# Optimization experiments

Hardware: AMD Instinct MI355X
Metric: run time of the kernel (lower is better)

The kernel has to match this reference:

```python
import jax, jax.numpy as jnp
import numpy as np

VOXEL = 0.1          # superpoint_voxel_size
NUM_BATCHES = 4      # B (batch indices in coords[:,0] are in [0, B))


def setup_inputs() -> dict:
    key = jax.random.key(0)
    k1, k2, k3, k4, k5, k6, k7 = jax.random.split(key, 7)
    N, D = 1_000_000, 64
    batch_ids = jax.random.randint(k1, (N,), 0, NUM_BATCHES).astype(jnp.float32)
    xyz = jax.random.uniform(k2, (N, 3), dtype=jnp.float32) * 50.0  # 50m scene
    coords = jnp.concatenate([batch_ids[:, None], xyz], axis=1)      # (N,4)
    features = jax.random.normal(k3, (N, D), dtype=jnp.float32)
    s1 = 1.0 / np.sqrt(3.0)
    s2 = 1.0 / np.sqrt(D)
    W1 = jax.random.uniform(k4, (3, D), minval=-s1, maxval=s1, dtype=jnp.float32)
    b1 = jax.random.uniform(k5, (D,), minval=-s1, maxval=s1, dtype=jnp.float32)
    W2 = jax.random.uniform(k6, (D, D), minval=-s2, maxval=s2, dtype=jnp.float32)
    b2 = jax.random.uniform(k7, (D,), minval=-s2, maxval=s2, dtype=jnp.float32)
    return {"coords": coords, "features": features, "W1": W1, "b1": b1, "W2": W2, "b2": b2}


def reference(coords, features, W1, b1, W2, b2):
    N, D = features.shape
    batch_ids = coords[:, 0].astype(jnp.int32)          # (N,)
    xyz = coords[:, 1:4]                                 # (N,3)
    q = jnp.floor(xyz / VOXEL).astype(jnp.int32)         # voxel quantization
    combined = jnp.concatenate([batch_ids[:, None], q], axis=1)  # (N,4) int32 keys

    # torch.unique(dim=0, return_inverse=True): lexicographically sorted unique
    # rows. We pad to a fixed S=N segments (fill rows sorted to the tail via a
    # max sentinel); `valid` masks out the padding.
    SENT = jnp.iinfo(jnp.int32).max
    unique_sp, sp_to_point = jnp.unique(
        combined, axis=0, size=N, fill_value=SENT, return_inverse=True)
    sp_to_point = sp_to_point.reshape(-1)                # (N,)

    counts = jax.ops.segment_sum(jnp.ones((N,), jnp.float32), sp_to_point, num_segments=N)
    valid = counts > 0
    c = jnp.maximum(counts, 1.0)[:, None]                # clamp(min=1)

    sp_features = jax.ops.segment_sum(features, sp_to_point, num_segments=N) / c  # (N,D) mean
    sp_centers = jax.ops.segment_sum(xyz, sp_to_point, num_segments=N) / c        # (N,3) mean

    # pos_enc: Linear(3,D) -> ReLU -> Linear(D,D)
    pos = jnp.maximum(sp_centers @ W1 + b1, 0.0) @ W2 + b2
    sp_features = jnp.where(valid[:, None], sp_features + pos, 0.0)
    sp_centers = jnp.where(valid[:, None], sp_centers, 0.0)

    # batch_offsets: cumulative superpoint counts per batch (padding -> dump bin B)
    sp_batch = jnp.where(valid, unique_sp[:, 0], NUM_BATCHES)
    per_batch = jax.ops.segment_sum(jnp.ones((N,), jnp.int32), sp_batch,
                                    num_segments=NUM_BATCHES + 1)[:NUM_BATCHES]
    batch_offsets = jnp.concatenate([jnp.zeros((1,), jnp.int32), jnp.cumsum(per_batch)])
    return sp_features, sp_centers, sp_to_point, batch_offsets
```

## Files before the change

### kernel.cpp

```cpp
#include <hip/hip_runtime.h>
#include <stdint.h>


static constexpr uint32_t NWORDS = 1u << 24;
static constexpr uint32_t NBLK   = NWORDS / 1024;
static constexpr uint32_t MCAP   = 65536;

typedef __attribute__((ext_vector_type(8))) short short8;
typedef __attribute__((ext_vector_type(4))) float f32x4;

__device__ __forceinline__ short f2bf(float x) {
    union { float f; uint32_t u; } v; v.f = x;
    uint32_t u = v.u;
    uint32_t r = (u + 0x7FFFu + ((u >> 16) & 1u)) >> 16;
    return (short)r;
}

__device__ __forceinline__ uint32_t point_key(float4 c) {
    uint32_t b  = (uint32_t)(int)c.x;
    uint32_t qx = (uint32_t)(int)floorf(c.y / 0.1f);
    uint32_t qy = (uint32_t)(int)floorf(c.z / 0.1f);
    uint32_t qz = (uint32_t)(int)floorf(c.w / 0.1f);
    return (b << 27) | (qx << 18) | (qy << 9) | qz;
}

__global__ void k0_w2t(const float* __restrict__ W2, short* __restrict__ W2T) {
    int t = blockIdx.x * 256 + threadIdx.x;
    if (t < 4096) {
        int col = t >> 6, k = t & 63;
        W2T[col * 64 + k] = f2bf(W2[k * 64 + col]);
    }
}

__global__ void k1_keys(const float4* __restrict__ coords, uint32_t* __restrict__ bitmap, int N) {
    int i = blockIdx.x * blockDim.x + threadIdx.x;
    if (i >= N) return;
    uint32_t key = point_key(coords[i]);
    atomicOr(&bitmap[key >> 5], 1u << (key & 31u));
}

__global__ __launch_bounds__(256) void k2a_blockscan(
        const uint4* __restrict__ bm4, uint16_t* __restrict__ scan4,
        uint32_t* __restrict__ bsum) {
    int t = threadIdx.x;
    int lane = t & 63, wid = t >> 6;
    uint4 v = bm4[(size_t)blockIdx.x * 256 + t];
    uint32_t pc = __popc(v.x) + __popc(v.y) + __popc(v.z) + __popc(v.w);
    uint32_t sc = pc;
    #pragma unroll
    for (int off = 1; off < 64; off <<= 1) {
        uint32_t n = __shfl_up(sc, off);
        if (lane >= off) sc += n;
    }
    __shared__ uint32_t wt[4];
    if (lane == 63) wt[wid] = sc;
    __syncthreads();
    uint32_t wbase = 0;
    #pragma unroll
    for (int w = 0; w < 4; ++w) wbase += (w < wid) ? wt[w] : 0u;
    scan4[(size_t)blockIdx.x * 256 + t] = (uint16_t)(wbase + sc - pc);
    if (t == 255) bsum[blockIdx.x] = wbase + sc;
}

__global__ void k2b_topscan(const uint32_t* __restrict__ bsum, uint32_t* __restrict__ bscan) {
    __shared__ uint32_t s[1024];
    int t = threadIdx.x;
    uint32_t base = (uint32_t)t * 16u;
    const uint4* b4 = (const uint4*)(bsum + base);
    uint32_t sum = 0;
    #pragma unroll
    for (int k = 0; k < 4; ++k) { uint4 v = b4[k]; sum += v.x + v.y + v.z + v.w; }
    s[t] = sum;
    __syncthreads();
    for (int off = 1; off < 1024; off <<= 1) {
        uint32_t v = (t >= off) ? s[t - off] : 0u;
        __syncthreads();
        s[t] += v;
        __syncthreads();
    }
    uint32_t run = s[t] - sum;
    for (int k = 0; k < 16; ++k) { bscan[base + k] = run; run += bsum[base + k]; }
    if (t == 1023) bscan[16384] = run;
}

__global__ void k3a_rank(const float4* __restrict__ coords,
                         uint32_t* __restrict__ ranks,
                         const uint32_t* __restrict__ bitmap,
                         const uint16_t* __restrict__ scan4,
                         const uint32_t* __restrict__ bscan,
                         float* __restrict__ psum,
                         uint32_t* __restrict__ mctr,
                         float* __restrict__ msum,
                         float* __restrict__ mfeat,
                         float* __restrict__ out_sp, int N) {
    int i = blockIdx.x * blockDim.x + threadIdx.x;
    if (i >= N) return;
    float4 c = coords[i];
    uint32_t key = point_key(c);
    uint32_t w = key >> 5, bit = key & 31u;
    uint4 q = *(const uint4*)(bitmap + (w & ~3u));
    uint32_t wd[4] = {q.x, q.y, q.z, q.w};
    uint32_t idx = w & 3u;
    uint32_t r = bscan[w >> 10] + (uint32_t)scan4[w >> 2];
    uint32_t cur = 0;
    #pragma unroll
    for (uint32_t j = 0; j < 4; ++j) {
        r += (j < idx) ? __popc(wd[j]) : 0u;
        cur = (j == idx) ? wd[j] : cur;
    }
    r += __popc(cur & ((1u << bit) - 1u));
    ranks[i] = r;
    out_sp[i] = (float)r;
    float* p = psum + 8u * (size_t)r;
    float old = atomicAdd(p, 1.0f);
    *(float4*)(p + 4) = make_float4(c.y, c.z, c.w, __uint_as_float((uint32_t)i));
    if (old == 1.0f) {
        uint32_t slot = atomicAdd(mctr, 1u);
        if (slot < MCAP) {
            *(uint32_t*)(p + 1) = slot + 1u;
            float4 z = make_float4(0.f, 0.f, 0.f, 0.f);
            *(float4*)(msum + 4u * (size_t)slot) = z;
            float4* fz = (float4*)(mfeat + 64u * (size_t)slot);
            #pragma unroll
            for (int qq = 0; qq < 16; ++qq) fz[qq] = z;
        }
    }
}

__global__ void k3fix(const float4* __restrict__ coords,
                      const float* __restrict__ features,
                      const uint32_t* __restrict__ ranks,
                      const float4* __restrict__ psum4,
                      float* __restrict__ msum,
                      float* __restrict__ mfeat, int N) {
    int i = blockIdx.x * blockDim.x + threadIdx.x;
    if (i >= N) return;
    uint32_t r = ranks[i];
    float4 q0 = psum4[2 * (size_t)r];
    uint32_t sl = __float_as_uint(q0.y);
    if (sl == 0) return;
    sl -= 1u;
    float cnt = q0.x;
    float4 c = coords[i];
    float* m = msum + 4u * (size_t)sl;
    atomicAdd(m + 0, c.y);
    atomicAdd(m + 1, c.z);
    atomicAdd(m + 2, c.w);
    float iv = 1.0f / cnt;
    const float* frow = features + (size_t)i * 64;
    float* orow = mfeat + (size_t)sl * 64;
    #pragma unroll 1
    for (int qq = 0; qq < 64; ++qq) atomicAdd(&orow[qq], frow[qq] * iv);
}

__global__ __launch_bounds__(256) void k5_fused(
        const f32x4* __restrict__ features4,
        const float4* __restrict__ psum4,
        const float4* __restrict__ msum,
        const f32x4* __restrict__ mfeat4,
        const float* __restrict__ W1, const float* __restrict__ b1,
        const short* __restrict__ W2T, const float* __restrict__ b2,
        f32x4* __restrict__ out_feat4, float* __restrict__ out_cent, int N) {
    int lane = threadIdx.x & 63;
    int rows_base = blockIdx.x * 256 + (threadIdx.x >> 6) * 64;

    float cntg[4], scx[4], scy[4], scz[4];
    uint32_t invg[4], slotg[4];
    #pragma unroll
    for (int g = 0; g < 4; ++g) {
        int rg = rows_base + (g << 4) + (lane & 15);
        int rgc = rg < N ? rg : N - 1;
        float4 q0 = psum4[2 * (size_t)rgc];
        float4 q1 = psum4[2 * (size_t)rgc + 1];
        float cnt = q0.x;
        cntg[g] = cnt;
        slotg[g] = __float_as_uint(q0.y);
        invg[g] = __float_as_uint(q1.w);
        float sx = q1.x, sy = q1.y, sz = q1.z;
        if (cnt > 1.5f) {
            float4 m = msum[slotg[g] - 1u];
            sx = m.x; sy = m.y; sz = m.z;
        }
        float ic = cnt > 0.f ? 1.f / cnt : 0.f;
        scx[g] = sx * ic; scy[g] = sy * ic; scz[g] = sz * ic;
    }

    int my = rows_base + lane;
    if (my < N) {
        float4 q0 = psum4[2 * (size_t)my];
        float4 q1 = psum4[2 * (size_t)my + 1];
        float cnt = q0.x;
        float sx = q1.x, sy = q1.y, sz = q1.z;
        if (cnt > 1.5f) {
            float4 m = msum[__float_as_uint(q0.y) - 1u];
            sx = m.x; sy = m.y; sz = m.z;
        }
        float ic = cnt > 0.f ? 1.f / cnt : 0.f;
        out_cent[3 * (size_t)my + 0] = sx * ic;
        out_cent[3 * (size_t)my + 1] = sy * ic;
        out_cent[3 * (size_t)my + 2] = sz * ic;
    }

    f32x4 acc[4][4];
    #pragma unroll
    for (int cg = 0; cg < 4; ++cg) {
        f32x4 bv = ((const f32x4*)b2)[(cg << 2) + (lane >> 4)];
        #pragma unroll
        for (int g = 0; g < 4; ++g)
            acc[g][cg] = bv;
    }

    #pragma unroll
    for (int s = 0; s < 2; ++s) {
        int kb = s * 32 + ((lane >> 4) << 3);
        float4 tx0 = *(const float4*)(W1 + kb),       tx1 = *(const float4*)(W1 + kb + 4);
        float4 ty0 = *(const float4*)(W1 + 64 + kb),  ty1 = *(const float4*)(W1 + 64 + kb + 4);
        float4 tz0 = *(const float4*)(W1 + 128 + kb), tz1 = *(const float4*)(W1 + 128 + kb + 4);
        float4 tb0 = *(const float4*)(b1 + kb),       tb1 = *(const float4*)(b1 + kb + 4);
        float w1x[8] = {tx0.x, tx0.y, tx0.z, tx0.w, tx1.x, tx1.y, tx1.z, tx1.w};
        float w1y[8] = {ty0.x, ty0.y, ty0.z, ty0.w, ty1.x, ty1.y, ty1.z, ty1.w};
        float w1z[8] = {tz0.x, tz0.y, tz0.z, tz0.w, tz1.x, tz1.y, tz1.z, tz1.w};
        float b1v[8] = {tb0.x, tb0.y, tb0.z, tb0.w, tb1.x, tb1.y, tb1.z, tb1.w};

        short8 afrag[4];
        #pragma unroll
        for (int cg = 0; cg < 4; ++cg) {
            int col = (cg << 4) | (lane & 15);
            afrag[cg] = *(const short8*)(W2T + col * 64 + kb);
        }

        #pragma unroll
        for (int g = 0; g < 4; ++g) {
            short8 hf;
            #pragma unroll
            for (int j = 0; j < 8; ++j) {
                float h = fmaf(scz[g], w1z[j], fmaf(scy[g], w1y[j], fmaf(scx[g], w1x[j], b1v[j])));
                hf[j] = f2bf(fmaxf(h, 0.0f));
            }
            #pragma unroll
            for (int cg = 0; cg < 4; ++cg)
                acc[g][cg] = __builtin_amdgcn_mfma_f32_16x16x32_bf16(afrag[cg], hf, acc[g][cg], 0, 0, 0);
        }
    }

    #pragma unroll
    for (int g = 0; g < 4; ++g) {
        int gr = rows_base + (g << 4) + (lane & 15);
        if (gr >= N) continue;
        float cnt = cntg[g];
        f32x4 v[4];
        #pragma unroll
        for (int cg = 0; cg < 4; ++cg) v[cg] = acc[g][cg];
        if (cnt == 0.0f) {
            #pragma unroll
            for (int cg = 0; cg < 4; ++cg) v[cg] = (f32x4){0.f, 0.f, 0.f, 0.f};
        } else if (cnt == 1.0f) {
            size_t fb = (size_t)invg[g] * 16 + (lane >> 4);
            #pragma unroll
            for (int cg = 0; cg < 4; ++cg) v[cg] += features4[fb + (cg << 2)];
        } else {
            size_t mb = (size_t)(slotg[g] - 1u) * 16 + (lane >> 4);
            #pragma unroll
            for (int cg = 0; cg < 4; ++cg) v[cg] += mfeat4[mb + (cg << 2)];
        }
        size_t ob = (size_t)gr * 16 + (lane >> 4);
        #pragma unroll
        for (int cg = 0; cg < 4; ++cg)
            out_feat4[ob + (cg << 2)] = v[cg];
    }
}

__global__ void k6_offsets(const uint32_t* __restrict__ bscan, float* __restrict__ out_off) {
    int t = threadIdx.x;
    if (t < 5) {
        uint32_t v;
        if (t == 0)      v = 0u;
        else if (t == 4) v = bscan[16384];
        else             v = bscan[(uint32_t)t << 12];
        out_off[t] = (float)v;
    }
}

extern "C" void kernel_launch(void* const* d_in, const int* in_sizes, int n_in,
                              void* d_out, int out_size, void* d_ws, size_t ws_size,
                              hipStream_t stream) {
    const float4* coords = (const float4*)d_in[0];
    const float*  feats  = (const float*)d_in[1];
    const float*  W1 = (const float*)d_in[2];
    const float*  b1 = (const float*)d_in[3];
    const float*  W2 = (const float*)d_in[4];
    const float*  b2 = (const float*)d_in[5];
    int N = in_sizes[0] / 4;

    char* ws = (char*)d_ws;
    size_t o = 0;
    uint32_t* bitmap = (uint32_t*)(ws + o); o += (size_t)NWORDS * 4;
    uint16_t* scan4  = (uint16_t*)(ws + o); o += (size_t)(NWORDS / 4) * 2;
    uint32_t* bsum   = (uint32_t*)(ws + o); o += (size_t)NBLK * 4;
    uint32_t* bscan  = (uint32_t*)(ws + o); o += (size_t)(NBLK + 1) * 4;
    o = (o + 31) & ~(size_t)31;
    float*    psum   = (float*)(ws + o);    o += (size_t)N * 32;
    uint32_t* ranks  = (uint32_t*)(ws + o); o += (size_t)N * 4;
    o = (o + 15) & ~(size_t)15;
    short*    W2T    = (short*)(ws + o);    o += 8192;
    uint32_t* mctr   = (uint32_t*)(ws + o); o += 16;
    float*    msum   = (float*)(ws + o);    o += (size_t)MCAP * 16;
    float*    mfeat  = (float*)(ws + o);    o += (size_t)MCAP * 256;

    float* out_feat = (float*)d_out;
    float* out_cent = out_feat + (size_t)N * 64;
    float* out_sp   = out_cent + (size_t)N * 3;
    float* out_off  = out_sp + N;

    hipMemsetAsync(bitmap, 0, (size_t)NWORDS * 4, stream);
    hipMemsetAsync(psum, 0, (size_t)N * 32, stream);
    hipMemsetAsync(mctr, 0, 16, stream);

    int nb = (N + 255) / 256;
    k0_w2t<<<16, 256, 0, stream>>>(W2, W2T);
    k1_keys<<<nb, 256, 0, stream>>>(coords, bitmap, N);
    k2a_blockscan<<<NBLK, 256, 0, stream>>>((const uint4*)bitmap, scan4, bsum);
    k2b_topscan<<<1, 1024, 0, stream>>>(bsum, bscan);
    k3a_rank<<<nb, 256, 0, stream>>>(coords, ranks, bitmap, scan4, bscan, psum,
                                     mctr, msum, mfeat, out_sp, N);
    k3fix<<<nb, 256, 0, stream>>>(coords, feats, ranks, (const float4*)psum, msum, mfeat, N);
    k5_fused<<<nb, 256, 0, stream>>>((const f32x4*)feats, (const float4*)psum,
                                     (const float4*)msum, (const f32x4*)mfeat,
                                     W1, b1, W2T, b2, (f32x4*)out_feat, out_cent, N);
    k6_offsets<<<1, 64, 0, stream>>>(bscan, out_off);
}
```

Baseline: 337.3 us.

## Fuse multi-point scatter into point-order MLP kernel and scatter singleton outputs

Merges the k3fix accumulation pass into a point-ordered kernel that computes the positional MLP from each point's own coordinates and writes singleton superpoint rows directly to their rank position. A second kernel handles empty rows and the rare multi-point superpoints with a scalar per-wavefront MLP, and writes the centers. This removes one full pass over ranks and coords and makes feature reads sequential. In exchange, output writes become a scatter by rank, and the multi-point path uses slower scalar FP32 math.

```diff
diff --git a/kernel.cpp b/kernel.cpp
--- a/kernel.cpp
+++ b/kernel.cpp
@@ -113,7 +113,7 @@
     out_sp[i] = (float)r;
     float* p = psum + 8u * (size_t)r;
     float old = atomicAdd(p, 1.0f);
-    *(float4*)(p + 4) = make_float4(c.y, c.z, c.w, __uint_as_float((uint32_t)i));
+    *(float4*)(p + 4) = make_float4(c.y, c.z, c.w, 0.f);
     if (old == 1.0f) {
         uint32_t slot = atomicAdd(mctr, 1u);
         if (slot < MCAP) {
@@ -127,78 +127,46 @@
     }
 }
 
-__global__ void k3fix(const float4* __restrict__ coords,
-                      const float* __restrict__ features,
-                      const uint32_t* __restrict__ ranks,
-                      const float4* __restrict__ psum4,
-                      float* __restrict__ msum,
-                      float* __restrict__ mfeat, int N) {
-    int i = blockIdx.x * blockDim.x + threadIdx.x;
-    if (i >= N) return;
-    uint32_t r = ranks[i];
-    float4 q0 = psum4[2 * (size_t)r];
-    uint32_t sl = __float_as_uint(q0.y);
-    if (sl == 0) return;
-    sl -= 1u;
-    float cnt = q0.x;
-    float4 c = coords[i];
-    float* m = msum + 4u * (size_t)sl;
-    atomicAdd(m + 0, c.y);
-    atomicAdd(m + 1, c.z);
-    atomicAdd(m + 2, c.w);
-    float iv = 1.0f / cnt;
-    const float* frow = features + (size_t)i * 64;
-    float* orow = mfeat + (size_t)sl * 64;
-    #pragma unroll 1
-    for (int qq = 0; qq < 64; ++qq) atomicAdd(&orow[qq], frow[qq] * iv);
-}
-
-__global__ __launch_bounds__(256) void k5_fused(
+__global__ __launch_bounds__(256) void k5a_scatter(
+        const float4* __restrict__ coords,
         const f32x4* __restrict__ features4,
+        const uint32_t* __restrict__ ranks,
         const float4* __restrict__ psum4,
-        const float4* __restrict__ msum,
-        const f32x4* __restrict__ mfeat4,
+        float* __restrict__ msum, float* __restrict__ mfeat,
         const float* __restrict__ W1, const float* __restrict__ b1,
         const short* __restrict__ W2T, const float* __restrict__ b2,
-        f32x4* __restrict__ out_feat4, float* __restrict__ out_cent, int N) {
+        f32x4* __restrict__ out_feat4, int N) {
     int lane = threadIdx.x & 63;
-    int rows_base = blockIdx.x * 256 + (threadIdx.x >> 6) * 64;
-
-    float cntg[4], scx[4], scy[4], scz[4];
-    uint32_t invg[4], slotg[4];
+    int base = blockIdx.x * 256 + (threadIdx.x >> 6) * 64;
+    int i = base + lane;
+    int icl = i < N ? i : N - 1;
+    float4 c = coords[icl];
+    uint32_t r = ranks[icl];
+    float4 q0 = psum4[2 * (size_t)r];
+    float cnt = q0.x;
+
+    if (i < N && cnt > 1.5f) {
+        uint32_t slw = __float_as_uint(q0.y);
+        if (slw) {
+            uint32_t sl = slw - 1u;
+            float* m = msum + 4u * (size_t)sl;
+            atomicAdd(m + 0, c.y);
+            atomicAdd(m + 1, c.z);
+            atomicAdd(m + 2, c.w);
+            float iv = 1.0f / cnt;
+            const float* frow = (const float*)(features4 + (size_t)icl * 16);
+            float* orow = mfeat + (size_t)sl * 64;
+            #pragma unroll 1
+            for (int qq = 0; qq < 64; ++qq) atomicAdd(&orow[qq], frow[qq] * iv);
+        }
+    }
+
+    float scx[4], scy[4], scz[4];
     #pragma unroll
     for (int g = 0; g < 4; ++g) {
-        int rg = rows_base + (g << 4) + (lane & 15);
-        int rgc = rg < N ? rg : N - 1;
-        float4 q0 = psum4[2 * (size_t)rgc];
-        float4 q1 = psum4[2 * (size_t)rgc + 1];
-        float cnt = q0.x;
-        cntg[g] = cnt;
-        slotg[g] = __float_as_uint(q0.y);
-        invg[g] = __float_as_uint(q1.w);
-        float sx = q1.x, sy = q1.y, sz = q1.z;
-        if (cnt > 1.5f) {
-            float4 m = msum[slotg[g] - 1u];
-            sx = m.x; sy = m.y; sz = m.z;
-        }
-        float ic = cnt > 0.f ? 1.f / cnt : 0.f;
-        scx[g] = sx * ic; scy[g] = sy * ic; scz[g] = sz * ic;
-    }
-
-    int my = rows_base + lane;
-    if (my < N) {
-        float4 q0 = psum4[2 * (size_t)my];
-        float4 q1 = psum4[2 * (size_t)my + 1];
-        float cnt = q0.x;
-        float sx = q1.x, sy = q1.y, sz = q1.z;
-        if (cnt > 1.5f) {
-            float4 m = msum[__float_as_uint(q0.y) - 1u];
-            sx = m.x; sy = m.y; sz = m.z;
-        }
-        float ic = cnt > 0.f ? 1.f / cnt : 0.f;
-        out_cent[3 * (size_t)my + 0] = sx * ic;
-        out_cent[3 * (size_t)my + 1] = sy * ic;
-        out_cent[3 * (size_t)my + 2] = sz * ic;
+        int pg = base + (g << 4) + (lane & 15);
+        float4 cc = coords[pg < N ? pg : N - 1];
+        scx[g] = cc.y; scy[g] = cc.z; scz[g] = cc.w;
     }
 
     f32x4 acc[4][4];
@@ -245,28 +213,69 @@
 
     #pragma unroll
     for (int g = 0; g < 4; ++g) {
-        int gr = rows_base + (g << 4) + (lane & 15);
-        if (gr >= N) continue;
-        float cnt = cntg[g];
-        f32x4 v[4];
-        #pragma unroll
-        for (int cg = 0; cg < 4; ++cg) v[cg] = acc[g][cg];
-        if (cnt == 0.0f) {
+        int src = (g << 4) | (lane & 15);
+        int prow = base + src;
+        float cr = __shfl(cnt, src);
+        uint32_t rr = (uint32_t)__shfl((int)r, src);
+        if (prow < N && cr == 1.0f) {
+            size_t fb = (size_t)prow * 16 + (lane >> 4);
+            size_t ob = (size_t)rr * 16 + (lane >> 4);
             #pragma unroll
-            for (int cg = 0; cg < 4; ++cg) v[cg] = (f32x4){0.f, 0.f, 0.f, 0.f};
-        } else if (cnt == 1.0f) {
-            size_t fb = (size_t)invg[g] * 16 + (lane >> 4);
-            #pragma unroll
-            for (int cg = 0; cg < 4; ++cg) v[cg] += features4[fb + (cg << 2)];
-        } else {
-            size_t mb = (size_t)(slotg[g] - 1u) * 16 + (lane >> 4);
-            #pragma unroll
-            for (int cg = 0; cg < 4; ++cg) v[cg] += mfeat4[mb + (cg << 2)];
-        }
-        size_t ob = (size_t)gr * 16 + (lane >> 4);
-        #pragma unroll
-        for (int cg = 0; cg < 4; ++cg)
-            out_feat4[ob + (cg << 2)] = v[cg];
+            for (int cg = 0; cg < 4; ++cg)
+                out_feat4[ob + (cg << 2)] = acc[g][cg] + features4[fb + (cg << 2)];
+        }
+    }
+}
+
+__global__ __launch_bounds__(256) void k5b_finish(
+        const float4* __restrict__ psum4,
+        const float4* __restrict__ msum,
+        const float* __restrict__ mfeat,
+        const float* __restrict__ W1, const float* __restrict__ b1,
+        const float* __restrict__ W2, const float* __restrict__ b2,
+        float* __restrict__ out_feat, float* __restrict__ out_cent, int N) {
+    int lane = threadIdx.x & 63;
+    int r = blockIdx.x * 256 + threadIdx.x;
+    int wrbase = blockIdx.x * 256 + (threadIdx.x & ~63);
+    int rcl = r < N ? r : N - 1;
+    float4 q0 = psum4[2 * (size_t)rcl];
+    float4 q1 = psum4[2 * (size_t)rcl + 1];
+    float cnt = r < N ? q0.x : 1.0f;
+    uint32_t slw = __float_as_uint(q0.y);
+
+    float cx = q1.x, cy = q1.y, cz = q1.z;
+    bool multi = (cnt > 1.5f) && (slw != 0u);
+    if (multi) {
+        float4 m = msum[slw - 1u];
+        float iv = 1.0f / cnt;
+        cx = m.x * iv; cy = m.y * iv; cz = m.z * iv;
+    }
+    if (r < N) {
+        bool valid = cnt > 0.0f;
+        out_cent[3 * (size_t)r + 0] = valid ? cx : 0.f;
+        out_cent[3 * (size_t)r + 1] = valid ? cy : 0.f;
+        out_cent[3 * (size_t)r + 2] = valid ? cz : 0.f;
+    }
+
+    unsigned long long zm = __ballot(r < N && cnt == 0.0f);
+    while (zm) {
+        int src = __ffsll(zm) - 1; zm &= zm - 1;
+        out_feat[(size_t)(wrbase + src) * 64 + lane] = 0.0f;
+    }
+
+    unsigned long long mm = __ballot(r < N && multi);
+    while (mm) {
+        int src = __ffsll(mm) - 1; mm &= mm - 1;
+        float mcx = __shfl(cx, src), mcy = __shfl(cy, src), mcz = __shfl(cz, src);
+        uint32_t msl = (uint32_t)__shfl((int)(slw - 1u), src);
+        float out = b2[lane];
+        #pragma unroll 1
+        for (int k = 0; k < 64; ++k) {
+            float hk = fmaxf(b1[k] + mcx * W1[k] + mcy * W1[64 + k] + mcz * W1[128 + k], 0.0f);
+            out = fmaf(hk, W2[64 * k + lane], out);
+        }
+        out += mfeat[(size_t)msl * 64 + lane];
+        out_feat[(size_t)(wrbase + src) * 64 + lane] = out;
     }
 }
 
@@ -323,9 +332,10 @@
     k2b_topscan<<<1, 1024, 0, stream>>>(bsum, bscan);
     k3a_rank<<<nb, 256, 0, stream>>>(coords, ranks, bitmap, scan4, bscan, psum,
                                      mctr, msum, mfeat, out_sp, N);
-    k3fix<<<nb, 256, 0, stream>>>(coords, feats, ranks, (const float4*)psum, msum, mfeat, N);
-    k5_fused<<<nb, 256, 0, stream>>>((const f32x4*)feats, (const float4*)psum,
-                                     (const float4*)msum, (const f32x4*)mfeat,
-                                     W1, b1, W2T, b2, (f32x4*)out_feat, out_cent, N);
+    k5a_scatter<<<nb, 256, 0, stream>>>(coords, (const f32x4*)feats, ranks,
+                                        (const float4*)psum, msum, mfeat,
+                                        W1, b1, W2T, b2, (f32x4*)out_feat, N);
+    k5b_finish<<<nb, 256, 0, stream>>>((const float4*)psum, (const float4*)msum,
+                                       mfeat, W1, b1, W2, b2, out_feat, out_cent, N);
     k6_offsets<<<1, 64, 0, stream>>>(bscan, out_off);
 }
```

Result: slower. 367.7 us (+9.0%).

## Compact multi-point voxels into a list so the fix-up kernel skips singletons

Applied to the files above, without the earlier changes.

The rank kernel now appends every point that lands in an already-occupied voxel to a compact list through an atomic counter, flagging the second arrival. The fix-up kernel walks only that list with a small grid-stride launch instead of reading ranks and psum for all N points. It also adds the first point's contribution via its stored index. The cost is an extra global atomic counter plus list writes, and possible contention on that counter. Correctness now depends on the first point's write racing with the second point's atomic.

```diff
diff --git a/kernel.cpp b/kernel.cpp
--- a/kernel.cpp
+++ b/kernel.cpp
@@ -89,9 +89,10 @@
                          const uint16_t* __restrict__ scan4,
                          const uint32_t* __restrict__ bscan,
                          float* __restrict__ psum,
-                         uint32_t* __restrict__ mctr,
+                         uint32_t* __restrict__ ctrs,
                          float* __restrict__ msum,
                          float* __restrict__ mfeat,
+                         uint2* __restrict__ mlist,
                          float* __restrict__ out_sp, int N) {
     int i = blockIdx.x * blockDim.x + threadIdx.x;
     if (i >= N) return;
@@ -113,44 +114,64 @@
     out_sp[i] = (float)r;
     float* p = psum + 8u * (size_t)r;
     float old = atomicAdd(p, 1.0f);
-    *(float4*)(p + 4) = make_float4(c.y, c.z, c.w, __uint_as_float((uint32_t)i));
-    if (old == 1.0f) {
-        uint32_t slot = atomicAdd(mctr, 1u);
-        if (slot < MCAP) {
-            *(uint32_t*)(p + 1) = slot + 1u;
-            float4 z = make_float4(0.f, 0.f, 0.f, 0.f);
-            *(float4*)(msum + 4u * (size_t)slot) = z;
-            float4* fz = (float4*)(mfeat + 64u * (size_t)slot);
-            #pragma unroll
-            for (int qq = 0; qq < 16; ++qq) fz[qq] = z;
-        }
-    }
-}
-
-__global__ void k3fix(const float4* __restrict__ coords,
-                      const float* __restrict__ features,
-                      const uint32_t* __restrict__ ranks,
-                      const float4* __restrict__ psum4,
-                      float* __restrict__ msum,
-                      float* __restrict__ mfeat, int N) {
-    int i = blockIdx.x * blockDim.x + threadIdx.x;
-    if (i >= N) return;
-    uint32_t r = ranks[i];
-    float4 q0 = psum4[2 * (size_t)r];
-    uint32_t sl = __float_as_uint(q0.y);
-    if (sl == 0) return;
-    sl -= 1u;
-    float cnt = q0.x;
-    float4 c = coords[i];
+    if (old == 0.0f) {
+        *(float4*)(p + 4) = make_float4(c.y, c.z, c.w, __uint_as_float((uint32_t)i));
+    } else {
+        bool alloc = (old == 1.0f);
+        if (alloc) {
+            uint32_t slot = atomicAdd(&ctrs[0], 1u);
+            if (slot < MCAP) {
+                *(uint32_t*)(p + 1) = slot + 1u;
+                float4 z = make_float4(0.f, 0.f, 0.f, 0.f);
+                *(float4*)(msum + 4u * (size_t)slot) = z;
+                float4* fz = (float4*)(mfeat + 64u * (size_t)slot);
+                #pragma unroll
+                for (int qq = 0; qq < 16; ++qq) fz[qq] = z;
+            }
+        }
+        uint32_t e = atomicAdd(&ctrs[1], 1u);
+        mlist[e] = make_uint2((uint32_t)i | (alloc ? 0x80000000u : 0u), r);
+    }
+}
+
+__device__ __forceinline__ void mf_add(const float4* coords, const float* features,
+                                       uint32_t pt, uint32_t sl, float iv,
+                                       float* msum, float* mfeat) {
+    float4 c = coords[pt];
     float* m = msum + 4u * (size_t)sl;
     atomicAdd(m + 0, c.y);
     atomicAdd(m + 1, c.z);
     atomicAdd(m + 2, c.w);
-    float iv = 1.0f / cnt;
-    const float* frow = features + (size_t)i * 64;
+    const float* frow = features + (size_t)pt * 64;
     float* orow = mfeat + (size_t)sl * 64;
     #pragma unroll 1
     for (int qq = 0; qq < 64; ++qq) atomicAdd(&orow[qq], frow[qq] * iv);
+}
+
+__global__ void k3fix(const float4* __restrict__ coords,
+                      const float* __restrict__ features,
+                      const uint2* __restrict__ mlist,
+                      const uint32_t* __restrict__ ctrs,
+                      const float4* __restrict__ psum4,
+                      float* __restrict__ msum, float* __restrict__ mfeat) {
+    uint32_t M = ctrs[1];
+    for (uint32_t t = blockIdx.x * blockDim.x + threadIdx.x; t < M;
+         t += gridDim.x * blockDim.x) {
+        uint2 e = mlist[t];
+        uint32_t i = e.x & 0x7FFFFFFFu;
+        bool alloc = (e.x >> 31) != 0u;
+        uint32_t r = e.y;
+        float4 q0 = psum4[2 * (size_t)r];
+        uint32_t slw = __float_as_uint(q0.y);
+        if (!slw) continue;
+        uint32_t sl = slw - 1u;
+        float iv = 1.0f / q0.x;
+        mf_add(coords, features, i, sl, iv, msum, mfeat);
+        if (alloc) {
+            uint32_t first = __float_as_uint(psum4[2 * (size_t)r + 1].w);
+            mf_add(coords, features, first, sl, iv, msum, mfeat);
+        }
+    }
 }
 
 __global__ __launch_bounds__(256) void k5_fused(
@@ -303,7 +324,8 @@
     uint32_t* ranks  = (uint32_t*)(ws + o); o += (size_t)N * 4;
     o = (o + 15) & ~(size_t)15;
     short*    W2T    = (short*)(ws + o);    o += 8192;
-    uint32_t* mctr   = (uint32_t*)(ws + o); o += 16;
+    uint32_t* ctrs   = (uint32_t*)(ws + o); o += 16;
+    uint2*    mlist  = (uint2*)(ws + o);    o += (size_t)N * 8;
     float*    msum   = (float*)(ws + o);    o += (size_t)MCAP * 16;
     float*    mfeat  = (float*)(ws + o);    o += (size_t)MCAP * 256;
 
@@ -314,7 +336,7 @@
 
     hipMemsetAsync(bitmap, 0, (size_t)NWORDS * 4, stream);
     hipMemsetAsync(psum, 0, (size_t)N * 32, stream);
-    hipMemsetAsync(mctr, 0, 16, stream);
+    hipMemsetAsync(ctrs, 0, 16, stream);
 
     int nb = (N + 255) / 256;
     k0_w2t<<<16, 256, 0, stream>>>(W2, W2T);
@@ -322,8 +344,9 @@
     k2a_blockscan<<<NBLK, 256, 0, stream>>>((const uint4*)bitmap, scan4, bsum);
     k2b_topscan<<<1, 1024, 0, stream>>>(bsum, bscan);
     k3a_rank<<<nb, 256, 0, stream>>>(coords, ranks, bitmap, scan4, bscan, psum,
-                                     mctr, msum, mfeat, out_sp, N);
-    k3fix<<<nb, 256, 0, stream>>>(coords, feats, ranks, (const float4*)psum, msum, mfeat, N);
+                                     ctrs, msum, mfeat, mlist, out_sp, N);
+    k3fix<<<64, 256, 0, stream>>>(coords, feats, mlist, ctrs, (const float4*)psum,
+                                  msum, mfeat);
     k5_fused<<<nb, 256, 0, stream>>>((const f32x4*)feats, (const float4*)psum,
                                      (const float4*)msum, (const f32x4*)mfeat,
                                      W1, b1, W2T, b2, (f32x4*)out_feat, out_cent, N);
```

After: 403.6 us. 1.2x slower.
